# Performance work log

Hardware: AMD Instinct MI355X
Metric: run time of the kernel (lower is better)

The kernel has to match this reference:

```python
import jax, jax.numpy as jnp
import numpy as np

K = 3          # number of nearest neighbors for interpolation
EPS = 1e-8     # inverse-distance epsilon
BN_EPS = 1e-5  # torch BatchNorm1d default eps

B, NY, NX = 4, 16384, 4096
CY, CX = 128, 256
DIM = CY + CX
SHARED = (512, 256, 128)


def setup_inputs() -> dict:
    key = jax.random.key(0)
    ks = jax.random.split(key, 16)
    inp = {
        'y_points': jax.random.normal(ks[0], (B, NY, 3), jnp.float32),
        'y_feats': jax.random.normal(ks[1], (B, NY, CY), jnp.float32),
        'x_points': jax.random.normal(ks[2], (B, NX, 3), jnp.float32),
        'x_feats': jax.random.normal(ks[3], (B, NX, CX), jnp.float32),
    }
    in_chs = (DIM,) + SHARED[:-1]
    for i, (cin, cout) in enumerate(zip(in_chs, SHARED), start=1):
        scale = 1.0 / np.sqrt(cin)
        inp[f'W{i}'] = jax.random.normal(ks[4 + i], (cout, cin), jnp.float32) * scale
        inp[f'b{i}'] = jnp.zeros((cout,), jnp.float32)
        inp[f'g{i}'] = jnp.ones((cout,), jnp.float32)
        inp[f'be{i}'] = jnp.zeros((cout,), jnp.float32)
    return inp


def _interpolate(y_points, x_points, y_feats, x_feats):
    # squared pairwise distances [B, Ny, Nx]
    d = (jnp.sum(y_points * y_points, -1)[:, :, None]
         + jnp.sum(x_points * x_points, -1)[:, None, :]
         - 2.0 * jnp.einsum('bnd,bmd->bnm', y_points, x_points))
    neg_d, idx = jax.lax.top_k(-d, K)             # K smallest distances
    dists = -neg_d                                 # [B, Ny, K]
    w = 1.0 / (dists + EPS)
    w = w / jnp.sum(w, -1, keepdims=True)
    # gather neighbor features: [B, Ny, K, Cx]
    nb = jnp.take_along_axis(x_feats[:, None, :, :], idx[..., None], axis=2)
    interp = jnp.sum(nb * w[..., None], axis=2)    # [B, Ny, Cx]
    return jnp.concatenate([y_feats, interp], axis=-1)


def _conv_bn_relu(y, W, b, g, beta):
    # 1x1 Conv1d == per-point linear; y: [B, Cin, N]
    y = jnp.einsum('oc,bcn->bon', W, y) + b[None, :, None]
    mu = jnp.mean(y, axis=(0, 2), keepdims=True)
    var = jnp.var(y, axis=(0, 2), keepdims=True)
    y = (y - mu) * jax.lax.rsqrt(var + BN_EPS)
    return jax.nn.relu(y * g[None, :, None] + beta[None, :, None])


def reference(y_points, y_feats, x_points, x_feats,
              W1, b1, g1, be1, W2, b2, g2, be2, W3, b3, g3, be3):
    i_points = _interpolate(y_points, x_points, y_feats, x_feats)  # [B, Ny, DIM]
    y = jnp.transpose(i_points, (0, 2, 1))                          # [B, DIM, Ny]
    y = _conv_bn_relu(y, W1, b1, g1, be1)
    y = _conv_bn_relu(y, W2, b2, g2, be2)
    y = _conv_bn_relu(y, W3, b3, g3, be3)
    return y
```

## Files before the change

kernel.cpp:

```cpp
#include <hip/hip_runtime.h>

#define NYTOT 16384
#define NXP 4096
#define MTOT 65536
#define CYC 128
#define CXC 256
#define DIMC 384

typedef __attribute__((ext_vector_type(8))) _Float16 half8;
typedef __attribute__((ext_vector_type(4))) _Float16 half4;
typedef __attribute__((ext_vector_type(4))) float floatx4;
typedef __attribute__((ext_vector_type(2))) float floatx2;

using half_t = _Float16;

struct alignas(16) HF8 { half_t h[8]; };

__device__ __forceinline__ float fmed3(float a, float b, float c) {
  return __builtin_amdgcn_fmed3f(a, b, c);
}

__global__ __launch_bounds__(1024) void xq_prep(
    const float* __restrict__ x_points, float4* __restrict__ xq) {
#pragma clang fp contract(off)
  int j = blockIdx.x * 1024 + threadIdx.x;
  int b = j >> 12, jj = j & 4095;
  const float* p = x_points + (size_t)b * NXP * 3 + 3 * jj;
  float x0 = p[0], x1 = p[1], x2 = p[2];
  float sx = (x0 * x0 + x1 * x1) + x2 * x2;
  float4 v; v.x = x0; v.y = x1; v.z = x2; v.w = sx;
  xq[j] = v;
}

__global__ __launch_bounds__(1024, 8) void interp_kernel(
    const float* __restrict__ y_points, const float* __restrict__ y_feats,
    const float* __restrict__ x_feats, const float4* __restrict__ xq,
    half_t* __restrict__ A0) {
#pragma clang fp contract(off)
  __shared__ float pd[16][128][3];
  __shared__ int   pi[16][128][3];
  __shared__ float t2s[128];
  __shared__ float sw[3][128];
  __shared__ int   si[3][128];
  const int b = blockIdx.x >> 7;
  const int chunk = blockIdx.x & 127;
  const int t = threadIdx.x;
  const int lane = t & 63;
  const int seg = t >> 6;
  const int yloc = lane << 1;

  const float* yp = y_points + ((size_t)b * NYTOT + chunk * 128 + yloc) * 3;
  floatx2 Y0 = {yp[0], yp[3]};
  floatx2 Y1 = {yp[1], yp[4]};
  floatx2 Y2 = {yp[2], yp[5]};
  floatx2 SY = (Y0 * Y0 + Y1 * Y1) + Y2 * Y2;

  const float4* xqs = xq + (size_t)b * NXP;
  const int jb = __builtin_amdgcn_readfirstlane(seg * 256);

  floatx2 D0 = {1e30f, 1e30f}, D1 = D0, D2 = D0;
#pragma unroll 8
  for (int jj = 0; jj < 256; ++jj) {
    float4 p = xqs[jb + jj];
    floatx2 inner = (Y0 * p.x + Y1 * p.y) + Y2 * p.z;
    floatx2 d = (SY + p.w) - 2.0f * inner;
    D2.x = fmed3(d.x, D1.x, D2.x);  D2.y = fmed3(d.y, D1.y, D2.y);
    D1.x = fmed3(d.x, D0.x, D1.x);  D1.y = fmed3(d.y, D0.y, D1.y);
    D0.x = fminf(d.x, D0.x);        D0.y = fminf(d.y, D0.y);
  }
  pd[seg][yloc][0] = D0.x; pd[seg][yloc][1] = D1.x; pd[seg][yloc][2] = D2.x;
  pd[seg][yloc + 1][0] = D0.y; pd[seg][yloc + 1][1] = D1.y; pd[seg][yloc + 1][2] = D2.y;
  __syncthreads();

  if (t < 128) {
    float m0 = 1e30f, m1 = 1e30f, m2 = 1e30f;
#pragma unroll
    for (int s = 0; s < 16; ++s)
#pragma unroll
      for (int c = 0; c < 3; ++c) {
        float v = pd[s][t][c];
        m2 = fmed3(v, m1, m2);
        m1 = fmed3(v, m0, m1);
        m0 = fminf(v, m0);
      }
    t2s[t] = m2;
  }
  __syncthreads();

  const float t2a = t2s[yloc], t2b = t2s[yloc + 1];
  const float tmax = fmaxf(t2a, t2b);
  float e0a = 1e30f, e1a = 1e30f, e2a = 1e30f; int k0a = 0, k1a = 0, k2a = 0;
  float e0b = 1e30f, e1b = 1e30f, e2b = 1e30f; int k0b = 0, k1b = 0, k2b = 0;
#pragma unroll 4
  for (int jj = 0; jj < 256; ++jj) {
    float4 p = xqs[jb + jj];
    floatx2 inner = (Y0 * p.x + Y1 * p.y) + Y2 * p.z;
    floatx2 d = (SY + p.w) - 2.0f * inner;
    if (fminf(d.x, d.y) <= tmax) {
      int j = jb + jj;
      {
        float dv = d.x;
        bool l0 = dv < e0a, l1 = dv < e1a, l2 = dv < e2a;
        e2a = l1 ? e1a : (l2 ? dv : e2a);  k2a = l1 ? k1a : (l2 ? j : k2a);
        e1a = l0 ? e0a : (l1 ? dv : e1a);  k1a = l0 ? k0a : (l1 ? j : k1a);
        e0a = l0 ? dv : e0a;               k0a = l0 ? j : k0a;
      }
      {
        float dv = d.y;
        bool l0 = dv < e0b, l1 = dv < e1b, l2 = dv < e2b;
        e2b = l1 ? e1b : (l2 ? dv : e2b);  k2b = l1 ? k1b : (l2 ? j : k2b);
        e1b = l0 ? e0b : (l1 ? dv : e1b);  k1b = l0 ? k0b : (l1 ? j : k1b);
        e0b = l0 ? dv : e0b;               k0b = l0 ? j : k0b;
      }
    }
  }
  pd[seg][yloc][0] = e0a; pd[seg][yloc][1] = e1a; pd[seg][yloc][2] = e2a;
  pi[seg][yloc][0] = k0a; pi[seg][yloc][1] = k1a; pi[seg][yloc][2] = k2a;
  pd[seg][yloc + 1][0] = e0b; pd[seg][yloc + 1][1] = e1b; pd[seg][yloc + 1][2] = e2b;
  pi[seg][yloc + 1][0] = k0b; pi[seg][yloc + 1][1] = k1b; pi[seg][yloc + 1][2] = k2b;
  __syncthreads();

  if (t < 128) {
    float f0 = 1e30f, f1 = 1e30f, f2 = 1e30f;
    int m0i = 0, m1i = 0, m2i = 0;
#pragma unroll
    for (int s = 0; s < 16; ++s)
#pragma unroll
      for (int c = 0; c < 3; ++c) {
        float d = pd[s][t][c]; int j = pi[s][t][c];
        bool l0 = d < f0, l1 = d < f1, l2 = d < f2;
        f2 = l1 ? f1 : (l2 ? d : f2);  m2i = l1 ? m1i : (l2 ? j : m2i);
        f1 = l0 ? f0 : (l1 ? d : f1);  m1i = l0 ? m0i : (l1 ? j : m1i);
        f0 = l0 ? d : f0;              m0i = l0 ? j : m0i;
      }
    float w0 = 1.0f / (f0 + 1e-8f), w1 = 1.0f / (f1 + 1e-8f), w2 = 1.0f / (f2 + 1e-8f);
    float ws = (w0 + w1) + w2;
    sw[0][t] = w0 / ws; sw[1][t] = w1 / ws; sw[2][t] = w2 / ws;
    si[0][t] = m0i; si[1][t] = m1i; si[2][t] = m2i;
  }
  __syncthreads();

  const floatx4* xf4 = (const floatx4*)(x_feats + (size_t)b * NXP * CXC);
  const floatx4* yf4 = (const floatx4*)(y_feats + ((size_t)b * NYTOT + chunk * 128) * CYC);
  half_t* fb = A0 + ((size_t)b * NYTOT + chunk * 128) * DIMC;
  {
    const int q = t & 63;
    const int ysub = t >> 6;
    for (int y2 = ysub; y2 < 128; y2 += 16) {
      int j0 = si[0][y2], j1 = si[1][y2], j2 = si[2][y2];
      float a0 = sw[0][y2], a1 = sw[1][y2], a2 = sw[2][y2];
      floatx4 v0 = xf4[(size_t)j0 * 64 + q];
      floatx4 v1 = xf4[(size_t)j1 * 64 + q];
      floatx4 v2 = xf4[(size_t)j2 * 64 + q];
      half4 h;
#pragma unroll
      for (int e = 0; e < 4; ++e)
        h[e] = (half_t)fmaf(v2[e], a2, fmaf(v1[e], a1, v0[e] * a0));
      *(half4*)&fb[(size_t)y2 * DIMC + CYC + q * 4] = h;
    }
  }
  {
    const int q2 = t & 31;
    const int ysub2 = t >> 5;
    for (int y2 = ysub2; y2 < 128; y2 += 32) {
      floatx4 v = yf4[(size_t)y2 * 32 + q2];
      half4 h;
#pragma unroll
      for (int e = 0; e < 4; ++e) h[e] = (half_t)v[e];
      *(half4*)&fb[(size_t)y2 * DIMC + q2 * 4] = h;
    }
  }
}

__global__ __launch_bounds__(256) void wcvt_kernel(
    const float* __restrict__ W1, const float* __restrict__ W2,
    const float* __restrict__ W3, half_t* __restrict__ out) {
  int i = blockIdx.x * 256 + threadIdx.x;
  const float* src; half_t* dst; int j;
  if (i < 49152)      { src = W1; dst = out;          j = i; }
  else if (i < 81920) { src = W2; dst = out + 196608; j = i - 49152; }
  else                { src = W3; dst = out + 327680; j = i - 81920; }
  floatx4 v = ((const floatx4*)src)[j];
  half4 h;
#pragma unroll
  for (int e = 0; e < 4; ++e) h[e] = (half_t)v[e];
  ((half4*)dst)[j] = h;
}

template<int K, int O, bool FUSEA>
__global__ __launch_bounds__(256) void gemm_f16(
    const half_t* __restrict__ A, const half_t* __restrict__ Wh,
    const float* __restrict__ bias, half_t* __restrict__ C,
    float* __restrict__ sums, const float* __restrict__ ssA) {
  __shared__ __align__(16) short As[8][2][512];
  __shared__ __align__(16) short Bs[8][2][512];
  const int m0 = blockIdx.x * 128;
  const int n0 = blockIdx.y * 128;
  const int tid = threadIdx.x;
  const int lane = tid & 63;
  const int wid = tid >> 6;
  const int wm = wid >> 1, wn = wid & 1;
  const int lm = lane & 15;
  const int lk = (lane >> 4) * 8;
  floatx4 acc[4][4] = {};

  for (int k0 = 0; k0 < K; k0 += 64) {
    __syncthreads();
    if constexpr (FUSEA) {
#pragma unroll
      for (int c = 0; c < 4; ++c) {
        int id = wid * 4 + c;
        int sub = id >> 1;
        int ks = id & 1;
        const half_t* src = Wh + (size_t)(n0 + sub * 16 + lm) * K + (k0 + ks * 32 + lk);
        __builtin_amdgcn_global_load_lds(
            (const __attribute__((address_space(1))) void*)src,
            (__attribute__((address_space(3))) void*)&Bs[sub][ks][0], 16, 0, 0);
      }
      const int r = tid & 127;
      const int hh = tid >> 7;
      const half_t* arow = A + (size_t)(m0 + r) * K + k0 + hh * 32;
      half8 in[4];
#pragma unroll
      for (int g = 0; g < 4; ++g) in[g] = *(const half8*)&arow[g * 8];
#pragma unroll
      for (int g = 0; g < 4; ++g) {
        int kc = k0 + hh * 32 + g * 8;
        half8 h;
#pragma unroll
        for (int e = 0; e < 8; ++e) {
          float f = fmaxf((float)in[g][e] * ssA[kc + e] + ssA[K + kc + e], 0.f);
          h[e] = (half_t)f;
        }
        *(half8*)&As[r >> 4][hh][(g * 16 + (r & 15)) * 8] = h;
      }
    } else {
#pragma unroll
      for (int c = 0; c < 8; ++c) {
        int id = wid * 8 + c;
        int sub = (id >> 1) & 7;
        int ks = id & 1;
        const half_t* src = (id < 16)
            ? A  + (size_t)(m0 + sub * 16 + lm) * K + (k0 + ks * 32 + lk)
            : Wh + (size_t)(n0 + sub * 16 + lm) * K + (k0 + ks * 32 + lk);
        __builtin_amdgcn_global_load_lds(
            (const __attribute__((address_space(1))) void*)src,
            (__attribute__((address_space(3))) void*)(id < 16 ? &As[sub][ks][0]
                                                             : &Bs[sub][ks][0]),
            16, 0, 0);
      }
    }
    __syncthreads();
#pragma unroll
    for (int ks = 0; ks < 2; ++ks) {
      half8 af[4], bfm[4];
#pragma unroll
      for (int i = 0; i < 4; ++i) af[i] = *(const half8*)&As[wm * 4 + i][ks][lane * 8];
#pragma unroll
      for (int j = 0; j < 4; ++j) bfm[j] = *(const half8*)&Bs[wn * 4 + j][ks][lane * 8];
#pragma unroll
      for (int i = 0; i < 4; ++i)
#pragma unroll
        for (int j = 0; j < 4; ++j)
          acc[i][j] = __builtin_amdgcn_mfma_f32_16x16x32_f16(af[i], bfm[j], acc[i][j], 0, 0, 0);
    }
  }

#pragma unroll
  for (int j = 0; j < 4; ++j) {
    int nn = n0 + wn * 64 + j * 16 + lm;
    float bv = bias[nn];
    float psum = 0.f, psq = 0.f;
#pragma unroll
    for (int i = 0; i < 4; ++i) {
      int mr = m0 + wm * 64 + i * 16 + (lane >> 4) * 4;
#pragma unroll
      for (int rr = 0; rr < 4; ++rr) {
        float z = acc[i][j][rr] + bv;
        C[(size_t)(mr + rr) * O + nn] = (half_t)z;
        psum += z; psq += z * z;
      }
    }
    psum += __shfl_xor(psum, 16, 64); psq += __shfl_xor(psq, 16, 64);
    psum += __shfl_xor(psum, 32, 64); psq += __shfl_xor(psq, 32, 64);
    if ((lane >> 4) == 0) {
      atomicAdd(&sums[nn], psum);
      atomicAdd(&sums[O + nn], psq);
    }
  }
}

__global__ void finalize_kernel(const float* __restrict__ sums, const float* __restrict__ g,
                                const float* __restrict__ be, float* __restrict__ ss, int O) {
  int c = threadIdx.x;
  if (c < O) {
    const float invN = 1.0f / 65536.0f;
    float mean = sums[c] * invN;
    float var = sums[O + c] * invN - mean * mean;
    float sc = g[c] / sqrtf(var + 1e-5f);
    float sh = be[c] - mean * sc;
    if (!isfinite(sc) || !isfinite(sh)) { sc = 1.0f; sh = 0.0f; }
    ss[c] = sc;
    ss[O + c] = sh;
  }
}

__global__ __launch_bounds__(256) void bn_transpose_kernel(
    const half_t* __restrict__ Z3, const float* __restrict__ ss, float* __restrict__ out) {
  __shared__ float tile[64][129];
  const int r0 = blockIdx.x * 64;
  const int b = r0 >> 14;
  const int n0 = r0 & (NYTOT - 1);
  const int t = threadIdx.x;
  const int cl = t & 127, rl = t >> 7;
  for (int p = 0; p < 32; ++p) {
    int rr = p * 2 + rl;
    float v = (float)Z3[(size_t)(r0 + rr) * 128 + cl];
    tile[rr][cl] = fmaxf(v * ss[cl] + ss[128 + cl], 0.f);
  }
  __syncthreads();
  const int nl = t & 63, cj = t >> 6;
  for (int p = 0; p < 32; ++p) {
    int c = p * 4 + cj;
    out[(size_t)b * 128 * NYTOT + (size_t)c * NYTOT + n0 + nl] = tile[nl][c];
  }
}

extern "C" void kernel_launch(void* const* d_in, const int* in_sizes, int n_in,
                              void* d_out, int out_size, void* d_ws, size_t ws_size,
                              hipStream_t stream) {
  const float* y_points = (const float*)d_in[0];
  const float* y_feats  = (const float*)d_in[1];
  const float* x_points = (const float*)d_in[2];
  const float* x_feats  = (const float*)d_in[3];
  const float* W1 = (const float*)d_in[4];  const float* b1 = (const float*)d_in[5];
  const float* g1 = (const float*)d_in[6];  const float* be1 = (const float*)d_in[7];
  const float* W2 = (const float*)d_in[8];  const float* b2 = (const float*)d_in[9];
  const float* g2 = (const float*)d_in[10]; const float* be2 = (const float*)d_in[11];
  const float* W3 = (const float*)d_in[12]; const float* b3 = (const float*)d_in[13];
  const float* g3 = (const float*)d_in[14]; const float* be3 = (const float*)d_in[15];

  char* ws = (char*)d_ws;
  half_t* A0 = (half_t*)ws;
  half_t* z1 = (half_t*)(ws + 50331648);
  half_t* z2 = (half_t*)ws;
  half_t* z3 = (half_t*)(ws + 50331648);
  float4* xq = (float4*)(ws + 50331648);
  float* st = (float*)(ws + 117440512);
  half_t* W1h = (half_t*)d_out;
  half_t* W2h = W1h + 196608;
  half_t* W3h = W1h + 327680;
  hipMemsetAsync(st, 0, 1792 * sizeof(float), stream);

  xq_prep<<<16, 1024, 0, stream>>>(x_points, xq);
  wcvt_kernel<<<352, 256, 0, stream>>>(W1, W2, W3, W1h);
  interp_kernel<<<512, 1024, 0, stream>>>(y_points, y_feats, x_feats, xq, A0);

  gemm_f16<384, 512, false><<<dim3(512, 4), 256, 0, stream>>>(A0, W1h, b1, z1, st + 0, nullptr);
  finalize_kernel<<<1, 512, 0, stream>>>(st + 0, g1, be1, st + 1792, 512);

  gemm_f16<512, 256, true><<<dim3(512, 2), 256, 0, stream>>>(z1, W2h, b2, z2, st + 1024, st + 1792);
  finalize_kernel<<<1, 256, 0, stream>>>(st + 1024, g2, be2, st + 2816, 256);

  gemm_f16<256, 128, true><<<dim3(512, 1), 256, 0, stream>>>(z2, W3h, b3, z3, st + 1536, st + 2816);
  finalize_kernel<<<1, 128, 0, stream>>>(st + 1536, g3, be3, st + 3328, 128);

  bn_transpose_kernel<<<1024, 256, 0, stream>>>(z3, st + 3328, (float*)d_out);
}
```

Measured before the change: 531.5 us.

## Use 256x128 tiles with 512 threads and XCD-aware block swizzle for layers 1-2

Adds a new GEMM kernel that computes a 256-row by 128-column output tile per workgroup with 8 waves instead of 128x128 with 4 waves. Blocks are remapped so consecutive tiles land on the same XCD (blockIdx & 7 interleave), improving L2 reuse of A rows across N tiles. This halves redundant weight loads per row and improves reuse, at the cost of more LDS per block and possibly lower occupancy. Only the first two pointwise-conv GEMMs switch to it.

```diff
diff --git a/kernel.cpp b/kernel.cpp
--- a/kernel.cpp
+++ b/kernel.cpp
@@ -187,6 +187,114 @@
   ((half4*)dst)[j] = h;
 }
 
+template<int K, int O, int NTN, bool FUSEA>
+__global__ __launch_bounds__(512) void gemm256(
+    const half_t* __restrict__ A, const half_t* __restrict__ Wh,
+    const float* __restrict__ bias, half_t* __restrict__ C,
+    float* __restrict__ sums, const float* __restrict__ ssA) {
+  __shared__ __align__(16) short As[16][2][512];
+  __shared__ __align__(16) short Bs[8][2][512];
+  constexpr int NWG = (MTOT / 256) * NTN;
+  const int lin = (blockIdx.x & 7) * (NWG >> 3) + (blockIdx.x >> 3);
+  const int m0 = (lin / NTN) * 256;
+  const int n0 = (lin % NTN) * 128;
+  const int tid = threadIdx.x;
+  const int lane = tid & 63;
+  const int wid = tid >> 6;
+  const int wm = wid >> 1, wn = wid & 1;
+  const int lm = lane & 15;
+  const int lk = (lane >> 4) * 8;
+  floatx4 acc[4][4] = {};
+
+  for (int k0 = 0; k0 < K; k0 += 64) {
+    __syncthreads();
+    if constexpr (FUSEA) {
+#pragma unroll
+      for (int c = 0; c < 2; ++c) {
+        int id = wid * 2 + c;
+        int sub = id >> 1, ks = id & 1;
+        const half_t* src = Wh + (size_t)(n0 + sub * 16 + lm) * K + (k0 + ks * 32 + lk);
+        __builtin_amdgcn_global_load_lds(
+            (const __attribute__((address_space(1))) void*)src,
+            (__attribute__((address_space(3))) void*)&Bs[sub][ks][0], 16, 0, 0);
+      }
+      const int r = tid & 255;
+      const int hh = tid >> 8;
+      const half_t* arow = A + (size_t)(m0 + r) * K + k0 + hh * 32;
+      half8 in[4];
+#pragma unroll
+      for (int g = 0; g < 4; ++g) in[g] = *(const half8*)&arow[g * 8];
+#pragma unroll
+      for (int g = 0; g < 4; ++g) {
+        int kc = k0 + hh * 32 + g * 8;
+        half8 h;
+#pragma unroll
+        for (int e = 0; e < 8; ++e) {
+          float f = fmaxf((float)in[g][e] * ssA[kc + e] + ssA[K + kc + e], 0.f);
+          h[e] = (half_t)f;
+        }
+        *(half8*)&As[r >> 4][hh][(g * 16 + (r & 15)) * 8] = h;
+      }
+    } else {
+#pragma unroll
+      for (int c = 0; c < 6; ++c) {
+        int id = wid * 6 + c;
+        if (id < 32) {
+          int sub = id >> 1, ks = id & 1;
+          const half_t* src = A + (size_t)(m0 + sub * 16 + lm) * K + (k0 + ks * 32 + lk);
+          __builtin_amdgcn_global_load_lds(
+              (const __attribute__((address_space(1))) void*)src,
+              (__attribute__((address_space(3))) void*)&As[sub][ks][0], 16, 0, 0);
+        } else {
+          int id2 = id - 32;
+          int sub = id2 >> 1, ks = id2 & 1;
+          const half_t* src = Wh + (size_t)(n0 + sub * 16 + lm) * K + (k0 + ks * 32 + lk);
+          __builtin_amdgcn_global_load_lds(
+              (const __attribute__((address_space(1))) void*)src,
+              (__attribute__((address_space(3))) void*)&Bs[sub][ks][0], 16, 0, 0);
+        }
+      }
+    }
+    __syncthreads();
+#pragma unroll
+    for (int ks = 0; ks < 2; ++ks) {
+      half8 af[4], bfm[4];
+#pragma unroll
+      for (int i = 0; i < 4; ++i) af[i] = *(const half8*)&As[wm * 4 + i][ks][lane * 8];
+#pragma unroll
+      for (int j = 0; j < 4; ++j) bfm[j] = *(const half8*)&Bs[wn * 4 + j][ks][lane * 8];
+#pragma unroll
+      for (int i = 0; i < 4; ++i)
+#pragma unroll
+        for (int j = 0; j < 4; ++j)
+          acc[i][j] = __builtin_amdgcn_mfma_f32_16x16x32_f16(af[i], bfm[j], acc[i][j], 0, 0, 0);
+    }
+  }
+
+#pragma unroll
+  for (int j = 0; j < 4; ++j) {
+    int nn = n0 + wn * 64 + j * 16 + lm;
+    float bv = bias[nn];
+    float psum = 0.f, psq = 0.f;
+#pragma unroll
+    for (int i = 0; i < 4; ++i) {
+      int mr = m0 + wm * 64 + i * 16 + (lane >> 4) * 4;
+#pragma unroll
+      for (int rr = 0; rr < 4; ++rr) {
+        float z = acc[i][j][rr] + bv;
+        C[(size_t)(mr + rr) * O + nn] = (half_t)z;
+        psum += z; psq += z * z;
+      }
+    }
+    psum += __shfl_xor(psum, 16, 64); psq += __shfl_xor(psq, 16, 64);
+    psum += __shfl_xor(psum, 32, 64); psq += __shfl_xor(psq, 32, 64);
+    if ((lane >> 4) == 0) {
+      atomicAdd(&sums[nn], psum);
+      atomicAdd(&sums[O + nn], psq);
+    }
+  }
+}
+
 template<int K, int O, bool FUSEA>
 __global__ __launch_bounds__(256) void gemm_f16(
     const half_t* __restrict__ A, const half_t* __restrict__ Wh,
@@ -356,10 +464,10 @@
   wcvt_kernel<<<352, 256, 0, stream>>>(W1, W2, W3, W1h);
   interp_kernel<<<512, 1024, 0, stream>>>(y_points, y_feats, x_feats, xq, A0);
 
-  gemm_f16<384, 512, false><<<dim3(512, 4), 256, 0, stream>>>(A0, W1h, b1, z1, st + 0, nullptr);
+  gemm256<384, 512, 4, false><<<1024, 512, 0, stream>>>(A0, W1h, b1, z1, st + 0, nullptr);
   finalize_kernel<<<1, 512, 0, stream>>>(st + 0, g1, be1, st + 1792, 512);
 
-  gemm_f16<512, 256, true><<<dim3(512, 2), 256, 0, stream>>>(z1, W2h, b2, z2, st + 1024, st + 1792);
+  gemm256<512, 256, 2, true><<<512, 512, 0, stream>>>(z1, W2h, b2, z2, st + 1024, st + 1792);
   finalize_kernel<<<1, 256, 0, stream>>>(st + 1024, g2, be2, st + 2816, 256);
 
   gemm_f16<256, 128, true><<<dim3(512, 1), 256, 0, stream>>>(z2, W3h, b3, z3, st + 1536, st + 2816);
```

After: 461.6 us. 1.15x faster.
